# Kernel optimization log

Hardware: AMD Instinct MI355X
Metric: run time of the kernel (lower is better)

The kernel has to match this reference:

```python
import jax, jax.numpy as jnp
import numpy as np

HIDDEN = 1024
HEADS = 16
HEAD_DIM = HIDDEN // HEADS


def setup_inputs() -> dict:
    key = jax.random.key(0)
    ks = jax.random.split(key, 10)
    B, S, D = 4, 2048, HIDDEN
    scale = 1.0 / np.sqrt(D)
    x = jax.random.normal(ks[0], (B, S, D), dtype=jnp.float32)
    mask = jax.random.bernoulli(ks[1], 0.1, (B, S))  # True = masked position
    Wq = jax.random.normal(ks[2], (D, D), dtype=jnp.float32) * scale
    Wk = jax.random.normal(ks[3], (D, D), dtype=jnp.float32) * scale
    Wv = jax.random.normal(ks[4], (D, D), dtype=jnp.float32) * scale
    Wo = jax.random.normal(ks[5], (D, D), dtype=jnp.float32) * scale
    bq = jnp.zeros((D,), jnp.float32)
    bk = jnp.zeros((D,), jnp.float32)
    bv = jnp.zeros((D,), jnp.float32)
    bo = jnp.zeros((D,), jnp.float32)
    return {"x": x, "mask": mask, "Wq": Wq, "bq": bq, "Wk": Wk, "bk": bk,
            "Wv": Wv, "bv": bv, "Wo": Wo, "bo": bo}


def reference(x, mask, Wq, bq, Wk, bk, Wv, bv, Wo, bo):
    B, S, D = x.shape
    H, dh = HEADS, HEAD_DIM
    # QKV projections -> [B, H, S, dh]
    def proj(W, b):
        return (x @ W + b).reshape(B, S, H, dh).transpose(0, 2, 1, 3)
    q, k, v = proj(Wq, bq), proj(Wk, bk), proj(Wv, bv)
    # scaled dot-product scores [B, H, S, S]
    scores = jnp.einsum("bhqd,bhkd->bhqk", q, k) / jnp.sqrt(jnp.asarray(dh, x.dtype))
    neg = jnp.finfo(x.dtype).min
    scores = jnp.where(mask[:, None, None, :], neg, scores)
    attn = jax.nn.softmax(scores, axis=-1)
    out = jnp.einsum("bhqk,bhkd->bhqd", attn, v)  # [B, H, S, dh]
    out = out.transpose(0, 2, 1, 3).reshape(B, S, D)
    return out @ Wo + bo  # dropout p=0.0 -> identity
```

## Files before the change

### kernel.cpp

```cpp
#include <hip/hip_runtime.h>
#include <hip/hip_bf16.h>

typedef __attribute__((ext_vector_type(8))) short bf8_t;
typedef __attribute__((ext_vector_type(4))) float f4_t;
typedef __attribute__((ext_vector_type(2))) unsigned int u2_t;
typedef __attribute__((ext_vector_type(4))) unsigned int u4_t;

#define MFMA16(a, b, c) __builtin_amdgcn_mfma_f32_16x16x32_bf16((a), (b), (c), 0, 0, 0)

static __device__ inline unsigned short f2bf(float f) {
    unsigned int u = __float_as_uint(f);
    unsigned int r = 0x7fffu + ((u >> 16) & 1u);
    return (unsigned short)((u + r) >> 16);
}

static __device__ inline float exp2_fast(float x) {
    float r;
    asm("v_exp_f32 %0, %1" : "=v"(r) : "v"(x));
    return r;
}

static __device__ inline unsigned int cvtpk_bf16(float lo, float hi) {
    unsigned int r;
    asm("v_cvt_pk_bf16_f32 %0, %1, %2" : "=v"(r) : "v"(lo), "v"(hi));
    return r;
}

static __device__ inline void gload16(const void* g, void* l) {
    __builtin_amdgcn_global_load_lds(
        (const __attribute__((address_space(1))) unsigned int*)g,
        (__attribute__((address_space(3))) unsigned int*)l, 16, 0, 0);
}

__global__ void k_bias(const void* __restrict__ maskp, float* __restrict__ fbias) {
    __shared__ int s_int, s_flt;
    const unsigned int* mw = (const unsigned int*)maskp;
    if (threadIdx.x == 0) { s_int = 1; s_flt = 1; }
    __syncthreads();
    int li = 1, lf = 1;
    for (int i = threadIdx.x; i < 2048; i += 1024) {
        unsigned int v = mw[i];
        if (v != 0u && v != 1u) li = 0;
        if (v != 0u && v != 0x3F800000u) lf = 0;
    }
    if (!li) atomicAnd(&s_int, 0);
    if (!lf) atomicAnd(&s_flt, 0);
    __syncthreads();
    const int flag = s_int ? 0 : (s_flt ? 1 : 2);
    const int*           mi = (const int*)maskp;
    const float*         mf = (const float*)maskp;
    const unsigned char* mb = (const unsigned char*)maskp;
    for (int i = threadIdx.x; i < 8192; i += 1024) {
        bool m = (flag == 0) ? (mi[i] != 0) : (flag == 1) ? (mf[i] != 0.0f) : (mb[i] != 0);
        fbias[i] = m ? -1e30f : 0.0f;
    }
}

__global__ void k_cvt(const float* __restrict__ x, unsigned short* __restrict__ xb, int n4) {
    int i = blockIdx.x * blockDim.x + threadIdx.x;
    if (i < n4) {
        float4 v = ((const float4*)x)[i];
        ushort4 o;
        o.x = f2bf(v.x); o.y = f2bf(v.y); o.z = f2bf(v.z); o.w = f2bf(v.w);
        ((ushort4*)xb)[i] = o;
    }
}

__global__ void k_transw(const float* __restrict__ Wq, const float* __restrict__ Wk,
                         const float* __restrict__ Wv, const float* __restrict__ Wo,
                         unsigned short* __restrict__ WT) {
    __shared__ float tile[32][33];
    const float* W = (blockIdx.z == 0) ? Wq : (blockIdx.z == 1) ? Wk : (blockIdx.z == 2) ? Wv : Wo;
    unsigned short* out = WT + (size_t)blockIdx.z * 1024 * 1024;
    int n_r = blockIdx.x * 32 + threadIdx.x;
    int k_r = blockIdx.y * 32 + threadIdx.y;
    #pragma unroll
    for (int j = 0; j < 32; j += 8)
        tile[threadIdx.y + j][threadIdx.x] = W[(size_t)(k_r + j) * 1024 + n_r];
    __syncthreads();
    int k_w = blockIdx.y * 32 + threadIdx.x;
    int n_w = blockIdx.x * 32 + threadIdx.y;
    #pragma unroll
    for (int j = 0; j < 32; j += 8)
        out[(size_t)(n_w + j) * 1024 + k_w] = f2bf(tile[threadIdx.x][threadIdx.y + j]);
}

template <int MODE>
__global__ __launch_bounds__(256) void k_gemm(
    const unsigned short* __restrict__ A,
    const unsigned short* __restrict__ WTb,
    const float* __restrict__ b0, const float* __restrict__ b1, const float* __restrict__ b2,
    void* __restrict__ outp, void* __restrict__ outp2)
{
    __shared__ __align__(16) unsigned short SH[32768];
    const int tid  = threadIdx.x;
    const int lane = tid & 63;
    const int w    = tid >> 6;
    const int wr   = w >> 1, wc = w & 1;
    const int lg   = lane >> 4, lr = lane & 15;
    const int lg4  = lg * 4;

    const int id   = blockIdx.x;
    const int xcd  = id & 7;
    const int j    = id >> 3;
    const int ncol = j >> 3;
    const int by   = xcd * 8 + (j & 7);
    const int z    = (MODE == 0) ? (ncol >> 3) : 0;
    const int bm   = by * 128;
    const int bn   = ((MODE == 0) ? (ncol & 7) : ncol) * 128;
    const unsigned short* WT = WTb + (MODE == 0 ? (size_t)z * (1024 * 1024) : 0);

    f4_t acc[4][4];
    const f4_t z4 = {0.f, 0.f, 0.f, 0.f};
    #pragma unroll
    for (int i = 0; i < 4; ++i)
        #pragma unroll
        for (int jj = 0; jj < 4; ++jj) acc[i][jj] = z4;

    int strow[4], stcol[4];
    #pragma unroll
    for (int p = 0; p < 4; ++p) {
        int o = p * 4096 + tid * 16;
        strow[p] = o >> 7;
        stcol[p] = (o & 127) ^ ((strow[p] & 7) << 4);
    }

    auto stage = [&](int buf, int k0) {
        char* base = (char*)SH + buf * 32768;
        #pragma unroll
        for (int p = 0; p < 4; ++p) {
            int o = p * 4096 + tid * 16;
            gload16((const char*)(A  + (size_t)(bm + strow[p]) * 1024 + k0) + stcol[p], base + o);
            gload16((const char*)(WT + (size_t)(bn + strow[p]) * 1024 + k0) + stcol[p], base + 16384 + o);
        }
    };

    const int swz = (lr & 7) << 4;
    auto compute = [&](int buf) {
        const char* base = (const char*)SH + buf * 32768;
        bf8_t af[2][4], bfv[2][4];
        #pragma unroll
        for (int kk = 0; kk < 2; ++kk) {
            int col = (kk * 64 + lg * 16) ^ swz;
            #pragma unroll
            for (int i = 0; i < 4; ++i)
                af[kk][i] = *(const bf8_t*)(base + (wr * 64 + i * 16 + lr) * 128 + col);
            #pragma unroll
            for (int jj = 0; jj < 4; ++jj)
                bfv[kk][jj] = *(const bf8_t*)(base + 16384 + (wc * 64 + jj * 16 + lr) * 128 + col);
        }
        __builtin_amdgcn_s_setprio(1);
        #pragma unroll
        for (int kk = 0; kk < 2; ++kk)
            #pragma unroll
            for (int i = 0; i < 4; ++i)
                #pragma unroll
                for (int jj = 0; jj < 4; ++jj)
                    acc[i][jj] = MFMA16(af[kk][i], bfv[kk][jj], acc[i][jj]);
        __builtin_amdgcn_s_setprio(0);
    };

    stage(0, 0);
    __syncthreads();

    #pragma unroll 1
    for (int tt = 0; tt < 8; ++tt) {
        stage(1, (2 * tt + 1) * 64);
        compute(0);
        __syncthreads();
        if (tt < 7) stage(0, (2 * tt + 2) * 64);
        compute(1);
        __syncthreads();
    }

    if (MODE == 0) {
        const float* bias = (z == 0) ? b0 : (z == 1) ? b1 : b2;
        const float sc = (z == 0) ? 0.18033688011112042f : 1.0f;
        const int bb = bm >> 11;
        const int sb = bm & 2047;

        if (z < 2) {
            #pragma unroll
            for (int i = 0; i < 4; ++i)
                #pragma unroll
                for (int jj = 0; jj < 4; ++jj) {
                    int c = wc * 64 + jj * 16 + lr;
                    float bcol = bias[bn + c];
                    #pragma unroll
                    for (int r = 0; r < 4; ++r) {
                        int s = wr * 64 + i * 16 + lg4 + r;
                        SH[s * 136 + c] = f2bf((acc[i][jj][r] + bcol) * sc);
                    }
                }
            __syncthreads();
            unsigned short* O = (unsigned short*)outp + (size_t)z * (8192 * 1024);
            #pragma unroll
            for (int it = 0; it < 8; ++it) {
                int idx = it * 256 + tid;
                int hh  = idx >> 10;
                int rem = idx & 1023;
                int ss  = rem >> 3;
                int cc  = rem & 7;
                u4_t v = *(const u4_t*)&SH[ss * 136 + hh * 64 + cc * 8];
                int hq = (bn >> 6) + hh;
                *(u4_t*)(O + (((size_t)(bb * 16 + hq)) * 2048 + sb + ss) * 64 + cc * 8) = v;
            }
        } else {
            #pragma unroll
            for (int i = 0; i < 4; ++i) {
                int spb = wr * 64 + 32 * (i >> 1) + 8 * lg + 4 * (i & 1);
                #pragma unroll
                for (int jj = 0; jj < 4; ++jj) {
                    int c = wc * 64 + jj * 16 + lr;
                    float bcol = bias[bn + c];
                    #pragma unroll
                    for (int r = 0; r < 4; ++r)
                        SH[c * 136 + spb + r] = f2bf(acc[i][jj][r] + bcol);
                }
            }
            __syncthreads();
            unsigned short* OT = (unsigned short*)outp2;
            #pragma unroll
            for (int it = 0; it < 8; ++it) {
                int idx  = it * 256 + tid;
                int drow = idx >> 4;
                int cc   = idx & 15;
                u4_t v = *(const u4_t*)&SH[drow * 136 + cc * 8];
                int dcol = bn + drow;
                int hq = dcol >> 6, dh = dcol & 63;
                *(u4_t*)(OT + (((size_t)(bb * 16 + hq)) * 64 + dh) * 2048 + sb + cc * 8) = v;
            }
        }
    } else {
        float* O = (float*)outp;
        float* SF = (float*)SH;
        #pragma unroll
        for (int hhalf = 0; hhalf < 2; ++hhalf) {
            if (wr == hhalf) {
                #pragma unroll
                for (int i = 0; i < 4; ++i)
                    #pragma unroll
                    for (int jj = 0; jj < 4; ++jj) {
                        int c = wc * 64 + jj * 16 + lr;
                        float bcol = b0[bn + c];
                        #pragma unroll
                        for (int r = 0; r < 4; ++r)
                            SF[(i * 16 + lg4 + r) * 132 + c] = acc[i][jj][r] + bcol;
                    }
            }
            __syncthreads();
            #pragma unroll
            for (int it = 0; it < 8; ++it) {
                int idx = it * 256 + tid;
                int ss  = idx >> 5;
                int cc  = idx & 31;
                u4_t v = *(const u4_t*)&SF[ss * 132 + cc * 4];
                *(u4_t*)(O + (size_t)(bm + hhalf * 64 + ss) * 1024 + bn + cc * 4) = v;
            }
            __syncthreads();
        }
    }
}

__global__ __launch_bounds__(256, 2) void k_attn(
    const unsigned short* __restrict__ Q,
    const unsigned short* __restrict__ K,
    const unsigned short* __restrict__ VT,
    const float* __restrict__ fbias,
    unsigned short* __restrict__ O)
{
    __shared__ __align__(16) unsigned short Kls[2][64][64];
    __shared__ __align__(16) unsigned short Vls[2][64][64];
    const int tid  = threadIdx.x;
    const int lane = tid & 63;
    const int w    = tid >> 6;
    const int lg   = lane >> 4, lr = lane & 15;
    const int lg4  = lg * 4;

    const int id = blockIdx.x;
    const int bh = (id & 7) * 8 + ((id >> 3) & 7);
    const int qt = id >> 6;
    const int b  = bh >> 4, h = bh & 15;
    const int q0 = qt * 256 + w * 64;
    const size_t base = (size_t)bh * (2048 * 64);

    const char* Kbase = (const char*)(K + base);
    const char* Vbase = (const char*)(VT + (size_t)bh * (64 * 2048));

    int srow[2], scol[2];
    #pragma unroll
    for (int p = 0; p < 2; ++p) {
        int o = p * 4096 + tid * 16;
        srow[p] = o >> 7;
        scol[p] = (o & 127) ^ ((srow[p] & 7) << 4);
    }

    auto stage = [&](int buf, int k0) {
        #pragma unroll
        for (int p = 0; p < 2; ++p) {
            int o = p * 4096 + tid * 16;
            gload16(Kbase + (size_t)(k0 + srow[p]) * 128 + scol[p],
                    (char*)&Kls[buf][0][0] + o);
            gload16(Vbase + (size_t)srow[p] * 4096 + (size_t)k0 * 2 + scol[p],
                    (char*)&Vls[buf][0][0] + o);
        }
    };

    bf8_t qf[4][2];
    #pragma unroll
    for (int sub = 0; sub < 4; ++sub) {
        const unsigned short* qp = Q + base + (size_t)(q0 + sub * 16 + lr) * 64 + lg * 8;
        qf[sub][0] = *(const bf8_t*)qp;
        qf[sub][1] = *(const bf8_t*)(qp + 32);
    }

    const f4_t z4 = {0.f, 0.f, 0.f, 0.f};
    f4_t oacc[4][4];
    #pragma unroll
    for (int sub = 0; sub < 4; ++sub)
        #pragma unroll
        for (int nf = 0; nf < 4; ++nf) oacc[sub][nf] = z4;
    f4_t lacc[4] = {z4, z4, z4, z4};

    u4_t uones = {0x3F803F80u, 0x3F803F80u, 0x3F803F80u, 0x3F803F80u};
    const bf8_t ones8 = __builtin_bit_cast(bf8_t, uones);

    const float* fb = fbias + b * 2048 + lg4;
    const int sw = (lr & 7) << 4;
    const int cA = (lg * 16) ^ sw;
    const int cB = (64 + lg * 16) ^ sw;
    const int vA = (16 * lg) ^ sw;
    const int vB = (64 + 16 * lg) ^ sw;

    auto sm = [&](f4_t (&s)[4], u4_t (&pf)[2]) {
        #pragma unroll
        for (int c2 = 0; c2 < 2; ++c2) {
            float e0 = exp2_fast(s[2*c2][0]);
            float e1 = exp2_fast(s[2*c2][1]);
            float e2 = exp2_fast(s[2*c2][2]);
            float e3 = exp2_fast(s[2*c2][3]);
            float e4 = exp2_fast(s[2*c2+1][0]);
            float e5 = exp2_fast(s[2*c2+1][1]);
            float e6 = exp2_fast(s[2*c2+1][2]);
            float e7 = exp2_fast(s[2*c2+1][3]);
            u4_t u;
            u.x = cvtpk_bf16(e0, e1);
            u.y = cvtpk_bf16(e2, e3);
            u.z = cvtpk_bf16(e4, e5);
            u.w = cvtpk_bf16(e6, e7);
            pf[c2] = u;
        }
    };

    auto tile_body = [&](int cur, int k0) {
        f4_t cb[4];
        #pragma unroll
        for (int mf = 0; mf < 4; ++mf)
            cb[mf] = *(const f4_t*)(fb + k0 + mf * 16);

        bf8_t kf[4][2];
        #pragma unroll
        for (int mf = 0; mf < 4; ++mf) {
            const char* kr = (const char*)&Kls[cur][mf * 16 + lr][0];
            kf[mf][0] = *(const bf8_t*)(kr + cA);
            kf[mf][1] = *(const bf8_t*)(kr + cB);
        }
        bf8_t vf[4][2];
        #pragma unroll
        for (int nf = 0; nf < 4; ++nf) {
            const char* vr = (const char*)&Vls[cur][nf * 16 + lr][0];
            vf[nf][0] = *(const bf8_t*)(vr + vA);
            vf[nf][1] = *(const bf8_t*)(vr + vB);
        }

        #pragma unroll
        for (int sub = 0; sub < 4; ++sub) {
            f4_t s[4];
            __builtin_amdgcn_s_setprio(1);
            #pragma unroll
            for (int mf = 0; mf < 4; ++mf)
                s[mf] = MFMA16(kf[mf][1], qf[sub][1], MFMA16(kf[mf][0], qf[sub][0], cb[mf]));
            __builtin_amdgcn_s_setprio(0);

            u4_t pf[2];
            sm(s, pf);

            __builtin_amdgcn_s_setprio(1);
            #pragma unroll
            for (int c = 0; c < 2; ++c) {
                bf8_t pb = __builtin_bit_cast(bf8_t, pf[c]);
                lacc[sub] = MFMA16(ones8, pb, lacc[sub]);
                #pragma unroll
                for (int nf = 0; nf < 4; ++nf)
                    oacc[sub][nf] = MFMA16(vf[nf][c], pb, oacc[sub][nf]);
            }
            __builtin_amdgcn_s_setprio(0);
        }
    };

    stage(0, 0);
    __syncthreads();

    #pragma unroll 1
    for (int tt = 0; tt < 16; ++tt) {
        stage(1, (2 * tt + 1) * 64);
        tile_body(0, 2 * tt * 64);
        __syncthreads();
        if (tt < 15) stage(0, (2 * tt + 2) * 64);
        tile_body(1, (2 * tt + 1) * 64);
        __syncthreads();
    }

    #pragma unroll
    for (int sub = 0; sub < 4; ++sub) {
        float inv = 1.0f / lacc[sub][0];
        int qrow = q0 + sub * 16 + lr;
        size_t ob = ((size_t)(b * 2048 + qrow)) * 1024 + h * 64 + lg4;
        #pragma unroll
        for (int nf = 0; nf < 4; ++nf) {
            u2_t uo;
            uo.x = cvtpk_bf16(oacc[sub][nf][0] * inv, oacc[sub][nf][1] * inv);
            uo.y = cvtpk_bf16(oacc[sub][nf][2] * inv, oacc[sub][nf][3] * inv);
            *(u2_t*)(O + ob + nf * 16) = uo;
        }
    }
}

extern "C" void kernel_launch(void* const* d_in, const int* in_sizes, int n_in,
                              void* d_out, int out_size, void* d_ws, size_t ws_size,
                              hipStream_t stream) {
    const float* x  = (const float*)d_in[0];
    const void*  mask = d_in[1];
    const float* Wq = (const float*)d_in[2];
    const float* bq = (const float*)d_in[3];
    const float* Wk = (const float*)d_in[4];
    const float* bk = (const float*)d_in[5];
    const float* Wv = (const float*)d_in[6];
    const float* bv = (const float*)d_in[7];
    const float* Wo = (const float*)d_in[8];
    const float* bo = (const float*)d_in[9];

    char* ws = (char*)d_ws;
    float*          fbias = (float*)(ws + 1024);
    unsigned short* xb    = (unsigned short*)(ws + 65536);
    unsigned short* wT    = (unsigned short*)(ws + 65536 + 16777216);
    unsigned short* qkv   = (unsigned short*)(ws + 65536 + 25165824);
    unsigned short* attnb = (unsigned short*)(ws + 65536 + 75497472);

    unsigned short* Qb = qkv;
    unsigned short* Kb = qkv + 8388608;
    unsigned short* VT = qkv + 16777216;

    k_bias<<<1, 1024, 0, stream>>>(mask, fbias);
    k_cvt<<<8192, 256, 0, stream>>>(x, xb, 2097152);
    k_transw<<<dim3(32, 32, 4), dim3(32, 8), 0, stream>>>(Wq, Wk, Wv, Wo, wT);
    k_gemm<0><<<1536, 256, 0, stream>>>(xb, wT, bq, bk, bv, (void*)qkv, (void*)VT);
    k_attn<<<512, 256, 0, stream>>>(Qb, Kb, VT, fbias, attnb);
    k_gemm<1><<<512, 256, 0, stream>>>(attnb, wT + 3145728, bo, bo, bo, d_out, nullptr);
}
```

Baseline: 163.9 us.

## Merge prep kernels into one launch and stage 128-key tiles in attention

Folds the mask-bias, x-to-bf16 conversion and weight-transpose kernels into a single k_prep launch dispatched by block index, removing two kernel launches and the gaps between them. The attention kernel now loads 128 keys per stage (two 64-key halves) with double buffering, which halves the number of __syncthreads barriers in the main loop. The LDS footprint of k_attn doubles to 64KB, which may reduce occupancy below the two blocks per CU targeted by its launch bounds. The mask-bias block now runs with 256 threads instead of 1024.

Measured after the change: 166.8 us. Within noise of the previous version (+1.8%).

```diff
diff --git a/kernel.cpp b/kernel.cpp
--- a/kernel.cpp
+++ b/kernel.cpp
@@ -32,57 +32,65 @@
         (__attribute__((address_space(3))) unsigned int*)l, 16, 0, 0);
 }
 
-__global__ void k_bias(const void* __restrict__ maskp, float* __restrict__ fbias) {
+__global__ __launch_bounds__(256) void k_prep(
+    const float* __restrict__ x, unsigned short* __restrict__ xb,
+    const float* __restrict__ Wq, const float* __restrict__ Wk,
+    const float* __restrict__ Wv, const float* __restrict__ Wo,
+    unsigned short* __restrict__ WT,
+    const void* __restrict__ maskp, float* __restrict__ fbias)
+{
+    __shared__ float tile[32][33];
     __shared__ int s_int, s_flt;
-    const unsigned int* mw = (const unsigned int*)maskp;
-    if (threadIdx.x == 0) { s_int = 1; s_flt = 1; }
-    __syncthreads();
-    int li = 1, lf = 1;
-    for (int i = threadIdx.x; i < 2048; i += 1024) {
-        unsigned int v = mw[i];
-        if (v != 0u && v != 1u) li = 0;
-        if (v != 0u && v != 0x3F800000u) lf = 0;
-    }
-    if (!li) atomicAnd(&s_int, 0);
-    if (!lf) atomicAnd(&s_flt, 0);
-    __syncthreads();
-    const int flag = s_int ? 0 : (s_flt ? 1 : 2);
-    const int*           mi = (const int*)maskp;
-    const float*         mf = (const float*)maskp;
-    const unsigned char* mb = (const unsigned char*)maskp;
-    for (int i = threadIdx.x; i < 8192; i += 1024) {
-        bool m = (flag == 0) ? (mi[i] != 0) : (flag == 1) ? (mf[i] != 0.0f) : (mb[i] != 0);
-        fbias[i] = m ? -1e30f : 0.0f;
-    }
-}
-
-__global__ void k_cvt(const float* __restrict__ x, unsigned short* __restrict__ xb, int n4) {
-    int i = blockIdx.x * blockDim.x + threadIdx.x;
-    if (i < n4) {
+    const int tid = threadIdx.x;
+    const int job = blockIdx.x;
+
+    if (job < 8192) {
+        int i = job * 256 + tid;
         float4 v = ((const float4*)x)[i];
         ushort4 o;
         o.x = f2bf(v.x); o.y = f2bf(v.y); o.z = f2bf(v.z); o.w = f2bf(v.w);
         ((ushort4*)xb)[i] = o;
-    }
-}
-
-__global__ void k_transw(const float* __restrict__ Wq, const float* __restrict__ Wk,
-                         const float* __restrict__ Wv, const float* __restrict__ Wo,
-                         unsigned short* __restrict__ WT) {
-    __shared__ float tile[32][33];
-    const float* W = (blockIdx.z == 0) ? Wq : (blockIdx.z == 1) ? Wk : (blockIdx.z == 2) ? Wv : Wo;
-    unsigned short* out = WT + (size_t)blockIdx.z * 1024 * 1024;
-    int n_r = blockIdx.x * 32 + threadIdx.x;
-    int k_r = blockIdx.y * 32 + threadIdx.y;
-    #pragma unroll
-    for (int j = 0; j < 32; j += 8)
-        tile[threadIdx.y + j][threadIdx.x] = W[(size_t)(k_r + j) * 1024 + n_r];
-    __syncthreads();
-    int k_w = blockIdx.y * 32 + threadIdx.x;
-    int n_w = blockIdx.x * 32 + threadIdx.y;
-    #pragma unroll
-    for (int j = 0; j < 32; j += 8)
-        out[(size_t)(n_w + j) * 1024 + k_w] = f2bf(tile[threadIdx.x][threadIdx.y + j]);
+    } else if (job < 12288) {
+        int jj = job - 8192;
+        int z  = jj >> 10;
+        int by = (jj >> 5) & 31;
+        int bx = jj & 31;
+        int tx = tid & 31, ty = tid >> 5;
+        const float* W = (z == 0) ? Wq : (z == 1) ? Wk : (z == 2) ? Wv : Wo;
+        unsigned short* out = WT + (size_t)z * 1024 * 1024;
+        int n_r = bx * 32 + tx;
+        int k_r = by * 32 + ty;
+        #pragma unroll
+        for (int j = 0; j < 32; j += 8)
+            tile[ty + j][tx] = W[(size_t)(k_r + j) * 1024 + n_r];
+        __syncthreads();
+        int k_w = by * 32 + tx;
+        int n_w = bx * 32 + ty;
+        #pragma unroll
+        for (int j = 0; j < 32; j += 8)
+            out[(size_t)(n_w + j) * 1024 + k_w] = f2bf(tile[tx][ty + j]);
+    } else {
+        const unsigned int* mw = (const unsigned int*)maskp;
+        if (tid == 0) { s_int = 1; s_flt = 1; }
+        __syncthreads();
+        int li = 1, lf = 1;
+        for (int i = tid; i < 2048; i += 256) {
+            unsigned int v = mw[i];
+            if (v != 0u && v != 1u) li = 0;
+            if (v != 0u && v != 0x3F800000u) lf = 0;
+        }
+        if (!li) atomicAnd(&s_int, 0);
+        if (!lf) atomicAnd(&s_flt, 0);
+        __syncthreads();
+        const int flag = s_int ? 0 : (s_flt ? 1 : 2);
+        const int*           mi = (const int*)maskp;
+        const float*         mf = (const float*)maskp;
+        const unsigned char* mb = (const unsigned char*)maskp;
+        for (int i = tid; i < 8192; i += 256) {
+            bool m = (flag == 0) ? (mi[i] != 0) : (flag == 1) ? (mf[i] != 0.0f) : (mb[i] != 0);
+            fbias[i] = m ? -1e30f : 0.0f;
+        }
+    }
 }
 
 template <int MODE>
@@ -269,8 +277,8 @@
     const float* __restrict__ fbias,
     unsigned short* __restrict__ O)
 {
-    __shared__ __align__(16) unsigned short Kls[2][64][64];
-    __shared__ __align__(16) unsigned short Vls[2][64][64];
+    __shared__ __align__(16) unsigned short Kls[2][2][64][64];
+    __shared__ __align__(16) unsigned short Vls[2][2][64][64];
     const int tid  = threadIdx.x;
     const int lane = tid & 63;
     const int w    = tid >> 6;
@@ -295,15 +303,19 @@
         scol[p] = (o & 127) ^ ((srow[p] & 7) << 4);
     }
 
-    auto stage = [&](int buf, int k0) {
+    auto stage_half = [&](int buf, int half, int k0h) {
         #pragma unroll
         for (int p = 0; p < 2; ++p) {
             int o = p * 4096 + tid * 16;
-            gload16(Kbase + (size_t)(k0 + srow[p]) * 128 + scol[p],
-                    (char*)&Kls[buf][0][0] + o);
-            gload16(Vbase + (size_t)srow[p] * 4096 + (size_t)k0 * 2 + scol[p],
-                    (char*)&Vls[buf][0][0] + o);
-        }
+            gload16(Kbase + (size_t)(k0h + srow[p]) * 128 + scol[p],
+                    (char*)&Kls[buf][half][0][0] + o);
+            gload16(Vbase + (size_t)srow[p] * 4096 + (size_t)k0h * 2 + scol[p],
+                    (char*)&Vls[buf][half][0][0] + o);
+        }
+    };
+    auto stage = [&](int buf, int k0) {
+        stage_half(buf, 0, k0);
+        stage_half(buf, 1, k0 + 64);
     };
 
     bf8_t qf[4][2];
@@ -352,7 +364,7 @@
         }
     };
 
-    auto tile_body = [&](int cur, int k0) {
+    auto tile_body = [&](int cur, int half, int k0) {
         f4_t cb[4];
         #pragma unroll
         for (int mf = 0; mf < 4; ++mf)
@@ -361,14 +373,14 @@
         bf8_t kf[4][2];
         #pragma unroll
         for (int mf = 0; mf < 4; ++mf) {
-            const char* kr = (const char*)&Kls[cur][mf * 16 + lr][0];
+            const char* kr = (const char*)&Kls[cur][half][mf * 16 + lr][0];
             kf[mf][0] = *(const bf8_t*)(kr + cA);
             kf[mf][1] = *(const bf8_t*)(kr + cB);
         }
         bf8_t vf[4][2];
         #pragma unroll
         for (int nf = 0; nf < 4; ++nf) {
-            const char* vr = (const char*)&Vls[cur][nf * 16 + lr][0];
+            const char* vr = (const char*)&Vls[cur][half][nf * 16 + lr][0];
             vf[nf][0] = *(const bf8_t*)(vr + vA);
             vf[nf][1] = *(const bf8_t*)(vr + vB);
         }
@@ -402,12 +414,14 @@
     __syncthreads();
 
     #pragma unroll 1
-    for (int tt = 0; tt < 16; ++tt) {
-        stage(1, (2 * tt + 1) * 64);
-        tile_body(0, 2 * tt * 64);
-        __syncthreads();
-        if (tt < 15) stage(0, (2 * tt + 2) * 64);
-        tile_body(1, (2 * tt + 1) * 64);
+    for (int tt = 0; tt < 8; ++tt) {
+        stage(1, (2 * tt + 1) * 128);
+        tile_body(0, 0, 2 * tt * 128);
+        tile_body(0, 1, 2 * tt * 128 + 64);
+        __syncthreads();
+        if (tt < 7) stage(0, (2 * tt + 2) * 128);
+        tile_body(1, 0, (2 * tt + 1) * 128);
+        tile_body(1, 1, (2 * tt + 1) * 128 + 64);
         __syncthreads();
     }
 
@@ -451,9 +465,7 @@
     unsigned short* Kb = qkv + 8388608;
     unsigned short* VT = qkv + 16777216;
 
-    k_bias<<<1, 1024, 0, stream>>>(mask, fbias);
-    k_cvt<<<8192, 256, 0, stream>>>(x, xb, 2097152);
-    k_transw<<<dim3(32, 32, 4), dim3(32, 8), 0, stream>>>(Wq, Wk, Wv, Wo, wT);
+    k_prep<<<12289, 256, 0, stream>>>(x, xb, Wq, Wk, Wv, Wo, wT, mask, fbias);
     k_gemm<0><<<1536, 256, 0, stream>>>(xb, wT, bq, bk, bv, (void*)qkv, (void*)VT);
     k_attn<<<512, 256, 0, stream>>>(Qb, Kb, VT, fbias, attnb);
     k_gemm<1><<<512, 256, 0, stream>>>(attnb, wT + 3145728, bo, bo, bo, d_out, nullptr);
```
